# Kernel optimization log

Hardware: AMD Instinct MI355X
Metric: run time of the kernel (lower is better)

## Reference

```python
import jax, jax.numpy as jnp
import numpy as np

N = 100_000   # nodes
E = 1_250_000 # edges
D = 64        # node feature dim
H = 64        # hidden_channels
C = 10        # num_classes
G = 128       # graphs in batch


def setup_inputs() -> dict:
    key = jax.random.key(0)
    ks = jax.random.split(key, 12)
    x = jax.random.normal(ks[0], (N, D), dtype=jnp.float32)
    edge_index = jax.random.randint(ks[1], (2, E), 0, N, dtype=jnp.int64)
    batch = jnp.sort(jax.random.randint(ks[2], (N,), 0, G, dtype=jnp.int64))
    s = lambda fan_in: 1.0 / np.sqrt(fan_in)
    W1 = jax.random.normal(ks[3], (D, H), dtype=jnp.float32) * s(D)
    b1 = jnp.zeros((H,), dtype=jnp.float32)
    W2 = jax.random.normal(ks[4], (H, H), dtype=jnp.float32) * s(H)
    b2 = jnp.zeros((H,), dtype=jnp.float32)
    W3 = jax.random.normal(ks[5], (H, H), dtype=jnp.float32) * s(H)
    b3 = jnp.zeros((H,), dtype=jnp.float32)
    Wl = jax.random.normal(ks[6], (H, C), dtype=jnp.float32) * s(H)
    bl = jnp.zeros((C,), dtype=jnp.float32)
    return {"x": x, "edge_index": edge_index, "batch": batch,
            "W1": W1, "b1": b1, "W2": W2, "b2": b2,
            "W3": W3, "b3": b3, "Wl": Wl, "bl": bl}


def _gcn_conv(h, W, b, src, dst, norm, n_nodes):
    # GCNConv: out[i] = sum_{e: dst(e)=i} norm_e * (h @ W)[src(e)] + b
    h = h @ W
    msg = h[src] * norm[:, None]                       # [E+N, H]
    return jax.ops.segment_sum(msg, dst, num_segments=n_nodes) + b


def reference(x, edge_index, batch, W1, b1, W2, b2, W3, b3, Wl, bl):
    x = x.astype(jnp.float32)
    ei = edge_index.astype(jnp.int64)
    # add self-loops (as PyG gcn_norm does by default)
    loop = jnp.arange(N, dtype=ei.dtype)
    src = jnp.concatenate([ei[0], loop])
    dst = jnp.concatenate([ei[1], loop])
    # symmetric normalization: deg over targets (in-degree incl. self-loops)
    deg = jax.ops.segment_sum(jnp.ones_like(src, dtype=jnp.float32), dst,
                              num_segments=N)
    dinv = jnp.where(deg > 0, jax.lax.rsqrt(jnp.maximum(deg, 1.0)), 0.0)
    norm = dinv[src] * dinv[dst]                       # [E+N]

    h = jax.nn.relu(_gcn_conv(x, W1, b1, src, dst, norm, N))
    h = jax.nn.relu(_gcn_conv(h, W2, b2, src, dst, norm, N))
    h = _gcn_conv(h, W3, b3, src, dst, norm, N)

    # global_mean_pool over graph ids
    ones = jnp.ones((N,), dtype=jnp.float32)
    counts = jax.ops.segment_sum(ones, batch, num_segments=G)
    sums = jax.ops.segment_sum(h, batch, num_segments=G)
    pooled = sums / jnp.maximum(counts, 1.0)[:, None]  # [G, H]

    # dropout is identity in eval mode
    return pooled @ Wl + bl                            # [G, C]
```

## Files before the change

### kernel.cpp

```cpp
#include <hip/hip_runtime.h>
#include <hip/hip_bf16.h>


#define BSHIFT 7
#define BNODES (1 << BSHIFT)
#define EPB    8192
#define MAXDEG 8192
#define MAXBUCKET 32768

typedef __attribute__((ext_vector_type(8))) short bf16x8;
typedef __attribute__((ext_vector_type(4))) float f32x4;

__device__ __forceinline__ void atomAddF(float* p, float v) {
#if defined(__gfx90a__) || defined(__gfx940__) || defined(__gfx941__) || defined(__gfx942__) || defined(__gfx950__)
    unsafeAtomicAdd(p, v);
#else
    atomicAdd(p, v);
#endif
}

__device__ __forceinline__ unsigned short f2bf(float x) {
    unsigned u = __float_as_uint(x);
    u += 0x7FFFu + ((u >> 16) & 1u);
    return (unsigned short)(u >> 16);
}
__device__ __forceinline__ float bf2f(unsigned short b) {
    return __uint_as_float((unsigned)b << 16);
}

__global__ __launch_bounds__(256)
void k_bhist(const int* __restrict__ dst, int* __restrict__ cnt_all,
             int nE, int nBuckets, int binBlocks,
             const float* __restrict__ W1, const float* __restrict__ W2,
             const float* __restrict__ W3, unsigned short* __restrict__ Wt,
             float* __restrict__ pool, int poolN) {
    if (blockIdx.x >= binBlocks) {
        int li = blockIdx.x - binBlocks;
        if (li < 3) {
            const float* W = (li == 0) ? W1 : ((li == 1) ? W2 : W3);
            unsigned short* o = Wt + li * 4096;
            for (int idx = threadIdx.x; idx < 4096; idx += 256) {
                int h = idx >> 6, k = idx & 63;
                o[idx] = f2bf(W[k * 64 + h]);
            }
        } else {
            for (int i = threadIdx.x; i < poolN; i += 256) pool[i] = 0.f;
        }
        return;
    }
    __shared__ int cnt[1024];
    const int t = threadIdx.x;
    const int blk = blockIdx.x * EPB;
    for (int b = t; b < nBuckets; b += 256) cnt[b] = 0;
    __syncthreads();
#pragma unroll 4
    for (int i = 0; i < EPB / 256; i++) {
        int e = blk + i * 256 + t;
        if (e < nE) atomicAdd(&cnt[dst[e] >> BSHIFT], 1);
    }
    __syncthreads();
    for (int b = t; b < nBuckets; b += 256)
        cnt_all[(size_t)blockIdx.x * nBuckets + b] = cnt[b];
}

__global__ __launch_bounds__(256)
void k_colscan(int* __restrict__ cnt_all, int* __restrict__ bcnt,
               int nBlocks, int nBuckets) {
    const int lane = threadIdx.x & 63;
    const int b = blockIdx.x * 4 + (threadIdx.x >> 6);
    if (b >= nBuckets) return;
    int running = 0;
    for (int c = 0; c < nBlocks; c += 64) {
        int blk = c + lane;
        int v = (blk < nBlocks) ? cnt_all[(size_t)blk * nBuckets + b] : 0;
        int incl = v;
#pragma unroll
        for (int off = 1; off < 64; off <<= 1) {
            int tv = __shfl_up(incl, off);
            if (lane >= off) incl += tv;
        }
        if (blk < nBlocks) cnt_all[(size_t)blk * nBuckets + b] = running + (incl - v);
        running += __shfl(incl, 63);
    }
    if (lane == 0) bcnt[b] = running;
}

__global__ void k_bscan(const int* __restrict__ bcnt, int* __restrict__ bbase,
                        int nb, int nE) {
    __shared__ int s[256];
    const int t = threadIdx.x;
    const int base = t * 4;
    int v0 = (base + 0 < nb) ? bcnt[base + 0] : 0;
    int v1 = (base + 1 < nb) ? bcnt[base + 1] : 0;
    int v2 = (base + 2 < nb) ? bcnt[base + 2] : 0;
    int v3 = (base + 3 < nb) ? bcnt[base + 3] : 0;
    int tsum = v0 + v1 + v2 + v3;
    s[t] = tsum;
    __syncthreads();
    for (int off = 1; off < 256; off <<= 1) {
        int val = 0;
        if (t >= off) val = s[t - off];
        __syncthreads();
        if (t >= off) s[t] += val;
        __syncthreads();
    }
    int excl = s[t] - tsum;
    if (base + 0 < nb) bbase[base + 0] = excl;
    if (base + 1 < nb) bbase[base + 1] = excl + v0;
    if (base + 2 < nb) bbase[base + 2] = excl + v0 + v1;
    if (base + 3 < nb) bbase[base + 3] = excl + v0 + v1 + v2;
    if (t == 0) bbase[nb] = nE;
}

__global__ __launch_bounds__(256)
void k_bucket(const int* __restrict__ src, const int* __restrict__ dst,
              const int* __restrict__ bbase, const int* __restrict__ cnt_all,
              int* __restrict__ staging, int nE, int nBuckets) {
    __shared__ int cnt[1024];
    __shared__ int lbase[1024];
    const int t = threadIdx.x;
    const int blk = blockIdx.x * EPB;

    for (int b = t; b < nBuckets; b += 256) {
        lbase[b] = bbase[b] + cnt_all[(size_t)blockIdx.x * nBuckets + b];
        cnt[b] = 0;
    }
    __syncthreads();
#pragma unroll 4
    for (int i = 0; i < EPB / 256; i++) {
        int e = blk + i * 256 + t;
        if (e < nE) {
            int s0 = src[e], d0 = dst[e];
            int b = d0 >> BSHIFT;
            int off = atomicAdd(&cnt[b], 1);
            int pos = lbase[b] + off;
            if ((unsigned)pos < (unsigned)nE)
                staging[pos] = (s0 << BSHIFT) | (d0 & (BNODES - 1));
        }
    }
}

__global__ __launch_bounds__(256)
void k_sort(const int* __restrict__ staging, const int* __restrict__ bbase,
            int* __restrict__ csr_s, int* __restrict__ rowptr,
            int* __restrict__ rowend, float* __restrict__ dinv,
            int n, int nE) {
    __shared__ int c[BNODES];
    __shared__ int sc[BNODES];
    __shared__ int cur[BNODES];
    const int t = threadIdx.x;
    const int b = blockIdx.x;
    const int node0 = b << BSHIFT;

    int seg0 = bbase[b];
    int seg1 = bbase[b + 1];
    seg0 = max(0, min(seg0, nE));
    seg1 = max(seg0, min(seg1, nE));
    seg1 = min(seg1, seg0 + MAXBUCKET);

    if (t < BNODES) c[t] = 0;
    __syncthreads();
    for (int e = seg0 + t; e < seg1; e += 256)
        atomicAdd(&c[staging[e] & (BNODES - 1)], 1);
    __syncthreads();
    if (t < BNODES) sc[t] = c[t];
    __syncthreads();
    for (int off = 1; off < BNODES; off <<= 1) {
        int v = 0;
        if (t >= off && t < BNODES) v = sc[t - off];
        __syncthreads();
        if (t >= off && t < BNODES) sc[t] += v;
        __syncthreads();
    }
    if (t < BNODES) {
        int excl = sc[t] - c[t];
        cur[t] = excl;
        int node = node0 + t;
        if (node < n) {
            rowptr[node] = seg0 + excl;
            rowend[node] = seg0 + excl + c[t];
            dinv[node]   = rsqrtf((float)c[t] + 1.0f);
        }
    }
    __syncthreads();
    for (int e = seg0 + t; e < seg1; e += 256) {
        int p = staging[e];
        int l = p & (BNODES - 1);
        int pos = seg0 + atomicAdd(&cur[l], 1);
        if ((unsigned)pos < (unsigned)nE)
            csr_s[pos] = ((unsigned)p) >> BSHIFT;
    }
}

template<bool RELU, typename AT>
__device__ __forceinline__
void gemm_body(int bid, const AT* __restrict__ in,
               const unsigned short* __restrict__ Wt,
               const float* __restrict__ bias,
               unsigned short* __restrict__ out, int n) {
    const int lane = threadIdx.x & 63;
    const int wid  = threadIdx.x >> 6;
    const int col  = lane & 15;
    const int quad = lane >> 4;
    const int node0w = bid * 64 + wid * 16;
    const int nodeA  = node0w + col;
    const bool validA = nodeA < n;

    f32x4 zero4 = {0.f, 0.f, 0.f, 0.f};
    f32x4 acc0 = zero4, acc1 = zero4, acc2 = zero4, acc3 = zero4;

#pragma unroll
    for (int ks = 0; ks < 64; ks += 32) {
        const int kb = ks + quad * 8;
        float a[8];
        if constexpr (sizeof(AT) == 4) {
            float4 a0 = make_float4(0.f, 0.f, 0.f, 0.f);
            float4 a1 = make_float4(0.f, 0.f, 0.f, 0.f);
            if (validA) {
                a0 = *(const float4*)((const float*)in + (size_t)nodeA * 64 + kb);
                a1 = *(const float4*)((const float*)in + (size_t)nodeA * 64 + kb + 4);
            }
            a[0] = a0.x; a[1] = a0.y; a[2] = a0.z; a[3] = a0.w;
            a[4] = a1.x; a[5] = a1.y; a[6] = a1.z; a[7] = a1.w;
        } else {
            ushort4 h0 = make_ushort4(0, 0, 0, 0), h1 = make_ushort4(0, 0, 0, 0);
            if (validA) {
                h0 = *(const ushort4*)((const unsigned short*)in + (size_t)nodeA * 64 + kb);
                h1 = *(const ushort4*)((const unsigned short*)in + (size_t)nodeA * 64 + kb + 4);
            }
            a[0] = bf2f(h0.x); a[1] = bf2f(h0.y); a[2] = bf2f(h0.z); a[3] = bf2f(h0.w);
            a[4] = bf2f(h1.x); a[5] = bf2f(h1.y); a[6] = bf2f(h1.z); a[7] = bf2f(h1.w);
        }
        if (RELU) {
#pragma unroll
            for (int i = 0; i < 8; i++) a[i] = fmaxf(a[i] + bias[kb + i], 0.f);
        }
        bf16x8 af;
#pragma unroll
        for (int i = 0; i < 8; i++) af[i] = (short)f2bf(a[i]);

        const bf16x8 b0f = *(const bf16x8*)(Wt + ((0 * 16 + col) * 64 + kb));
        const bf16x8 b1f = *(const bf16x8*)(Wt + ((1 * 16 + col) * 64 + kb));
        const bf16x8 b2f = *(const bf16x8*)(Wt + ((2 * 16 + col) * 64 + kb));
        const bf16x8 b3f = *(const bf16x8*)(Wt + ((3 * 16 + col) * 64 + kb));
        acc0 = __builtin_amdgcn_mfma_f32_16x16x32_bf16(af, b0f, acc0, 0, 0, 0);
        acc1 = __builtin_amdgcn_mfma_f32_16x16x32_bf16(af, b1f, acc1, 0, 0, 0);
        acc2 = __builtin_amdgcn_mfma_f32_16x16x32_bf16(af, b2f, acc2, 0, 0, 0);
        acc3 = __builtin_amdgcn_mfma_f32_16x16x32_bf16(af, b3f, acc3, 0, 0, 0);
    }

#pragma unroll
    for (int r = 0; r < 4; r++) {
        int nn = node0w + quad * 4 + r;
        if (nn < n) {
            size_t base = (size_t)nn * 64 + col;
            out[base +  0] = f2bf(acc0[r]);
            out[base + 16] = f2bf(acc1[r]);
            out[base + 32] = f2bf(acc2[r]);
            out[base + 48] = f2bf(acc3[r]);
        }
    }
}

template<bool RELU, typename AT>
__global__ __launch_bounds__(256)
void k_gemm(const AT* __restrict__ in, const unsigned short* __restrict__ Wt,
            const float* __restrict__ bias, unsigned short* __restrict__ out, int n) {
    gemm_body<RELU, AT>(blockIdx.x, in, Wt, bias, out, n);
}

__global__ __launch_bounds__(256)
void k_wfgemm1(const int* __restrict__ csr_s, const float* __restrict__ dinv,
               float* __restrict__ csr_w, int nE, int n, int wfB,
               const float* __restrict__ x, const unsigned short* __restrict__ Wt,
               unsigned short* __restrict__ hW) {
    if (blockIdx.x < wfB) {
        int e = blockIdx.x * 256 + threadIdx.x;
        if (e < nE) {
            int s = csr_s[e];
            s = max(0, min(s, n - 1));
            csr_w[e] = dinv[s];
        }
        return;
    }
    gemm_body<false, float>(blockIdx.x - wfB, x, Wt, nullptr, hW, n);
}

template<int LAYER>
__global__ __launch_bounds__(256)
void k_agg(const unsigned short* __restrict__ hW, const int* __restrict__ rowptr,
           const int* __restrict__ rowend, const int* __restrict__ csr_s,
           const float* __restrict__ csr_w, const float* __restrict__ dinv,
           unsigned short* __restrict__ aggb, int n, int nE) {
    const int lane = threadIdx.x & 63;
    const int wid  = threadIdx.x >> 6;
    const int nA = blockIdx.x * 8 + wid * 2;
    const int nB = nA + 1;
    if (nA >= n) return;
    const bool vB = (nB < n);

    int rowA = rowptr[nA], endA = rowend[nA];
    rowA = max(0, min(rowA, nE)); endA = max(rowA, min(endA, nE));
    endA = min(endA, rowA + MAXDEG);
    int rowB = 0, endB = 0;
    if (vB) {
        rowB = rowptr[nB]; endB = rowend[nB];
        rowB = max(0, min(rowB, nE)); endB = max(rowB, min(endB, nE));
        endB = min(endB, rowB + MAXDEG);
    }
    const float diA = dinv[nA];
    const float diB = vB ? dinv[nB] : 0.f;

    float a0 = diA * diA * bf2f(hW[(size_t)nA * 64 + lane]);
    float a1 = 0.f, a2 = 0.f, a3 = 0.f;
    float b0 = vB ? diB * diB * bf2f(hW[(size_t)nB * 64 + lane]) : 0.f;
    float b1 = 0.f, b2 = 0.f, b3 = 0.f;

    int baseA = rowA, baseB = rowB;
    while (baseA < endA || baseB < endB) {
        int mA = max(0, min(32, endA - baseA));
        int mB = max(0, min(32, endB - baseB));
        int   s_l = 0;
        float w_l = 0.f;
        if (lane < 32) {
            if (lane < mA) {
                int e = baseA + lane;
                s_l = csr_s[e];
                w_l = csr_w[e] * diA;
            }
        } else {
            int l2 = lane - 32;
            if (l2 < mB) {
                int e = baseB + l2;
                s_l = csr_s[e];
                w_l = csr_w[e] * diB;
            }
        }
        const int m = max(mA, mB);
        int j = 0;
        for (; j + 4 <= m; j += 4) {
            int   sA0 = __shfl(s_l, j),      sA1 = __shfl(s_l, j + 1);
            int   sA2 = __shfl(s_l, j + 2),  sA3 = __shfl(s_l, j + 3);
            int   sB0 = __shfl(s_l, j + 32), sB1 = __shfl(s_l, j + 33);
            int   sB2 = __shfl(s_l, j + 34), sB3 = __shfl(s_l, j + 35);
            float wA0 = __shfl(w_l, j),      wA1 = __shfl(w_l, j + 1);
            float wA2 = __shfl(w_l, j + 2),  wA3 = __shfl(w_l, j + 3);
            float wB0 = __shfl(w_l, j + 32), wB1 = __shfl(w_l, j + 33);
            float wB2 = __shfl(w_l, j + 34), wB3 = __shfl(w_l, j + 35);
            float hA0 = bf2f(hW[(size_t)sA0 * 64 + lane]);
            float hA1 = bf2f(hW[(size_t)sA1 * 64 + lane]);
            float hA2 = bf2f(hW[(size_t)sA2 * 64 + lane]);
            float hA3 = bf2f(hW[(size_t)sA3 * 64 + lane]);
            float hB0 = bf2f(hW[(size_t)sB0 * 64 + lane]);
            float hB1 = bf2f(hW[(size_t)sB1 * 64 + lane]);
            float hB2 = bf2f(hW[(size_t)sB2 * 64 + lane]);
            float hB3 = bf2f(hW[(size_t)sB3 * 64 + lane]);
            a0 += wA0 * hA0; a1 += wA1 * hA1;
            a2 += wA2 * hA2; a3 += wA3 * hA3;
            b0 += wB0 * hB0; b1 += wB1 * hB1;
            b2 += wB2 * hB2; b3 += wB3 * hB3;
        }
        for (; j < m; j++) {
            int   sA = __shfl(s_l, j);
            float wA = __shfl(w_l, j);
            int   sB = __shfl(s_l, j + 32);
            float wB = __shfl(w_l, j + 32);
            a0 += wA * bf2f(hW[(size_t)sA * 64 + lane]);
            b0 += wB * bf2f(hW[(size_t)sB * 64 + lane]);
        }
        baseA += mA;
        baseB += mB;
    }
    aggb[(size_t)nA * 64 + lane] = f2bf((a0 + a1) + (a2 + a3));
    if (vB) aggb[(size_t)nB * 64 + lane] = f2bf((b0 + b1) + (b2 + b3));
}

__global__ void k_pool(const unsigned short* __restrict__ aggb,
                       const int* __restrict__ batch,
                       float* __restrict__ pool, float* __restrict__ cnt, int n) {
    const int lane = threadIdx.x;
    const int base = blockIdx.x * 64;
    int g_cur = -1, run = 0;
    float acc = 0.f;
    for (int j = 0; j < 64; j++) {
        int node = base + j;
        if (node >= n) break;
        int g = batch[node];
        if (g != g_cur) {
            if (g_cur >= 0) {
                atomAddF(&pool[g_cur * 64 + lane], acc);
                if (lane == 0) atomAddF(&cnt[g_cur], (float)run);
            }
            g_cur = g; acc = 0.f; run = 0;
        }
        acc += bf2f(aggb[(size_t)node * 64 + lane]);
        run++;
    }
    if (g_cur >= 0) {
        atomAddF(&pool[g_cur * 64 + lane], acc);
        if (lane == 0) atomAddF(&cnt[g_cur], (float)run);
    }
}

__global__ void k_final(const float* __restrict__ pool, const float* __restrict__ cnt,
                        const float* __restrict__ b3, const float* __restrict__ Wl,
                        const float* __restrict__ bl, float* __restrict__ out) {
    __shared__ float s[64];
    const int g = blockIdx.x, t = threadIdx.x;
    float c = fmaxf(cnt[g], 1.0f);
    s[t] = pool[g * 64 + t] / c + b3[t];
    __syncthreads();
    if (t < 10) {
        float acc = bl[t];
#pragma unroll
        for (int k = 0; k < 64; k++) acc += s[k] * Wl[k * 10 + t];
        out[g * 10 + t] = acc;
    }
}

extern "C" void kernel_launch(void* const* d_in, const int* in_sizes, int n_in,
                              void* d_out, int out_size, void* d_ws, size_t ws_size,
                              hipStream_t stream) {
    const float* x   = (const float*)d_in[0];
    const int*   ei  = (const int*)d_in[1];
    const int*   bat = (const int*)d_in[2];
    const float* W1  = (const float*)d_in[3];
    const float* b1  = (const float*)d_in[4];
    const float* W2  = (const float*)d_in[5];
    const float* b2  = (const float*)d_in[6];
    const float* W3  = (const float*)d_in[7];
    const float* b3  = (const float*)d_in[8];
    const float* Wl  = (const float*)d_in[9];
    const float* bl  = (const float*)d_in[10];
    float* out = (float*)d_out;

    const int N_ = in_sizes[0] / 64;
    const int E_ = in_sizes[1] / 2;
    const int G_ = out_size / 10;
    const int NB_ = (N_ + BNODES - 1) >> BSHIFT;
    const int bin_blocks = (E_ + EPB - 1) / EPB;

    char* p = (char*)d_ws;
    int*   staging = (int*)p;   p += (size_t)E_ * 4;
    int*   csr_s  = (int*)p;    p += (size_t)E_ * 4;
    float* csr_w  = (float*)p;  p += (size_t)E_ * 4;
    unsigned short* aggb = (unsigned short*)p; p += (size_t)N_ * 64 * 2;
    unsigned short* hW   = (unsigned short*)p; p += (size_t)N_ * 64 * 2;
    float* dinv   = (float*)p;  p += (size_t)N_ * 4;
    int*   rowptr = (int*)p;    p += (size_t)N_ * 4;
    int*   rowend = (int*)p;    p += (size_t)N_ * 4;
    float* pool   = (float*)p;  p += (size_t)G_ * 64 * 4;
    float* cnt    = (float*)p;  p += (size_t)G_ * 4;
    unsigned short* Wt = (unsigned short*)p; p += 3 * 4096 * 2;
    int*   bcnt   = (int*)p;    p += (size_t)(NB_ + 1) * 4;
    int*   bbase  = (int*)p;    p += (size_t)(NB_ + 1) * 4;
    int*   cnt_all = (int*)p;   p += (size_t)bin_blocks * NB_ * 4;

    const int* srcp = ei;
    const int* dstp = ei + E_;

    k_bhist<<<bin_blocks + 4, 256, 0, stream>>>(dstp, cnt_all, E_, NB_,
                                                bin_blocks, W1, W2, W3, Wt,
                                                pool, G_ * 64 + G_);
    k_colscan<<<(NB_ + 3) / 4, 256, 0, stream>>>(cnt_all, bcnt, bin_blocks, NB_);
    k_bscan<<<1, 256, 0, stream>>>(bcnt, bbase, NB_, E_);
    k_bucket<<<bin_blocks, 256, 0, stream>>>(srcp, dstp, bbase, cnt_all,
                                             staging, E_, NB_);
    k_sort<<<NB_, 256, 0, stream>>>(staging, bbase, csr_s, rowptr, rowend,
                                    dinv, N_, E_);

    const int gemm_blocks = (N_ + 63) / 64;
    const int agg_blocks  = (N_ + 7) / 8;
    const int wf_blocks   = (E_ + 255) / 256;

    k_wfgemm1<<<wf_blocks + gemm_blocks, 256, 0, stream>>>(
        csr_s, dinv, csr_w, E_, N_, wf_blocks, x, Wt, hW);
    k_agg<1><<<agg_blocks, 256, 0, stream>>>(hW, rowptr, rowend, csr_s, csr_w,
                                             dinv, aggb, N_, E_);
    k_gemm<true, unsigned short><<<gemm_blocks, 256, 0, stream>>>(aggb, Wt + 4096,
                                                                  b1, hW, N_);
    k_agg<2><<<agg_blocks, 256, 0, stream>>>(hW, rowptr, rowend, csr_s, csr_w,
                                             dinv, aggb, N_, E_);
    k_gemm<true, unsigned short><<<gemm_blocks, 256, 0, stream>>>(aggb, Wt + 8192,
                                                                  b2, hW, N_);
    k_agg<3><<<agg_blocks, 256, 0, stream>>>(hW, rowptr, rowend, csr_s, csr_w,
                                             dinv, aggb, N_, E_);

    k_pool<<<(N_ + 63) / 64, 64, 0, stream>>>(aggb, bat, pool, cnt, N_);
    k_final<<<G_, 64, 0, stream>>>(pool, cnt, b3, Wl, bl, out);
}
```

Measured before the change: 345.9 us.

## Aggregate one node per wavefront using scalar constant-address edge loads

```diff
diff --git a/kernel.cpp b/kernel.cpp
--- a/kernel.cpp
+++ b/kernel.cpp
@@ -10,6 +10,13 @@
 
 typedef __attribute__((ext_vector_type(8))) short bf16x8;
 typedef __attribute__((ext_vector_type(4))) float f32x4;
+
+#define KAS __attribute__((address_space(4)))
+
+template <typename T>
+__device__ __forceinline__ const KAS T* kptr(const T* p) {
+    return (const KAS T*)(unsigned long long)p;
+}
 
 __device__ __forceinline__ void atomAddF(float* p, float v) {
 #if defined(__gfx90a__) || defined(__gfx940__) || defined(__gfx941__) || defined(__gfx942__) || defined(__gfx950__)
@@ -294,85 +301,48 @@
            unsigned short* __restrict__ aggb, int n, int nE) {
     const int lane = threadIdx.x & 63;
     const int wid  = threadIdx.x >> 6;
-    const int nA = blockIdx.x * 8 + wid * 2;
-    const int nB = nA + 1;
-    if (nA >= n) return;
-    const bool vB = (nB < n);
-
-    int rowA = rowptr[nA], endA = rowend[nA];
+    const int node = blockIdx.x * 4 + wid;
+    if (node >= n) return;
+
+    int rowA = __builtin_amdgcn_readfirstlane(rowptr[node]);
+    int endA = __builtin_amdgcn_readfirstlane(rowend[node]);
     rowA = max(0, min(rowA, nE)); endA = max(rowA, min(endA, nE));
     endA = min(endA, rowA + MAXDEG);
-    int rowB = 0, endB = 0;
-    if (vB) {
-        rowB = rowptr[nB]; endB = rowend[nB];
-        rowB = max(0, min(rowB, nE)); endB = max(rowB, min(endB, nE));
-        endB = min(endB, rowB + MAXDEG);
-    }
-    const float diA = dinv[nA];
-    const float diB = vB ? dinv[nB] : 0.f;
-
-    float a0 = diA * diA * bf2f(hW[(size_t)nA * 64 + lane]);
-    float a1 = 0.f, a2 = 0.f, a3 = 0.f;
-    float b0 = vB ? diB * diB * bf2f(hW[(size_t)nB * 64 + lane]) : 0.f;
-    float b1 = 0.f, b2 = 0.f, b3 = 0.f;
-
-    int baseA = rowA, baseB = rowB;
-    while (baseA < endA || baseB < endB) {
-        int mA = max(0, min(32, endA - baseA));
-        int mB = max(0, min(32, endB - baseB));
-        int   s_l = 0;
-        float w_l = 0.f;
-        if (lane < 32) {
-            if (lane < mA) {
-                int e = baseA + lane;
-                s_l = csr_s[e];
-                w_l = csr_w[e] * diA;
-            }
-        } else {
-            int l2 = lane - 32;
-            if (l2 < mB) {
-                int e = baseB + l2;
-                s_l = csr_s[e];
-                w_l = csr_w[e] * diB;
-            }
-        }
-        const int m = max(mA, mB);
-        int j = 0;
-        for (; j + 4 <= m; j += 4) {
-            int   sA0 = __shfl(s_l, j),      sA1 = __shfl(s_l, j + 1);
-            int   sA2 = __shfl(s_l, j + 2),  sA3 = __shfl(s_l, j + 3);
-            int   sB0 = __shfl(s_l, j + 32), sB1 = __shfl(s_l, j + 33);
-            int   sB2 = __shfl(s_l, j + 34), sB3 = __shfl(s_l, j + 35);
-            float wA0 = __shfl(w_l, j),      wA1 = __shfl(w_l, j + 1);
-            float wA2 = __shfl(w_l, j + 2),  wA3 = __shfl(w_l, j + 3);
-            float wB0 = __shfl(w_l, j + 32), wB1 = __shfl(w_l, j + 33);
-            float wB2 = __shfl(w_l, j + 34), wB3 = __shfl(w_l, j + 35);
-            float hA0 = bf2f(hW[(size_t)sA0 * 64 + lane]);
-            float hA1 = bf2f(hW[(size_t)sA1 * 64 + lane]);
-            float hA2 = bf2f(hW[(size_t)sA2 * 64 + lane]);
-            float hA3 = bf2f(hW[(size_t)sA3 * 64 + lane]);
-            float hB0 = bf2f(hW[(size_t)sB0 * 64 + lane]);
-            float hB1 = bf2f(hW[(size_t)sB1 * 64 + lane]);
-            float hB2 = bf2f(hW[(size_t)sB2 * 64 + lane]);
-            float hB3 = bf2f(hW[(size_t)sB3 * 64 + lane]);
-            a0 += wA0 * hA0; a1 += wA1 * hA1;
-            a2 += wA2 * hA2; a3 += wA3 * hA3;
-            b0 += wB0 * hB0; b1 += wB1 * hB1;
-            b2 += wB2 * hB2; b3 += wB3 * hB3;
-        }
-        for (; j < m; j++) {
-            int   sA = __shfl(s_l, j);
-            float wA = __shfl(w_l, j);
-            int   sB = __shfl(s_l, j + 32);
-            float wB = __shfl(w_l, j + 32);
-            a0 += wA * bf2f(hW[(size_t)sA * 64 + lane]);
-            b0 += wB * bf2f(hW[(size_t)sB * 64 + lane]);
-        }
-        baseA += mA;
-        baseB += mB;
-    }
-    aggb[(size_t)nA * 64 + lane] = f2bf((a0 + a1) + (a2 + a3));
-    if (vB) aggb[(size_t)nB * 64 + lane] = f2bf((b0 + b1) + (b2 + b3));
+    const float diA = __uint_as_float(
+        __builtin_amdgcn_readfirstlane(__float_as_uint(dinv[node])));
+
+    float acc0 = diA * bf2f(hW[(size_t)node * 64 + lane]);
+    float acc1 = 0.f, acc2 = 0.f, acc3 = 0.f;
+    const int nm1 = n - 1;
+
+    for (int b = rowA; b < endA; b += 16) {
+        const KAS int*   sp = kptr(csr_s + b);
+        const KAS float* wp = kptr(csr_w + b);
+        const int rem = endA - b;
+
+        int   sidx[16];
+        float w[16];
+#pragma unroll
+        for (int j = 0; j < 16; j++) {
+            int s = sp[j];
+            s = max(0, min(s, nm1));
+            sidx[j] = (j < rem) ? s : 0;
+            w[j]    = (j < rem) ? wp[j] : 0.f;
+        }
+        float h[16];
+#pragma unroll
+        for (int j = 0; j < 16; j++)
+            h[j] = bf2f(hW[(size_t)sidx[j] * 64 + lane]);
+#pragma unroll
+        for (int j = 0; j < 16; j += 4) {
+            acc0 += w[j]     * h[j];
+            acc1 += w[j + 1] * h[j + 1];
+            acc2 += w[j + 2] * h[j + 2];
+            acc3 += w[j + 3] * h[j + 3];
+        }
+    }
+    float r = diA * ((acc0 + acc1) + (acc2 + acc3));
+    aggb[(size_t)node * 64 + lane] = f2bf(r);
 }
 
 __global__ void k_pool(const unsigned short* __restrict__ aggb,
@@ -470,7 +440,7 @@
                                     dinv, N_, E_);
 
     const int gemm_blocks = (N_ + 63) / 64;
-    const int agg_blocks  = (N_ + 7) / 8;
+    const int agg_blocks  = (N_ + 3) / 4;
     const int wf_blocks   = (E_ + 255) / 256;
 
     k_wfgemm1<<<wf_blocks + gemm_blocks, 256, 0, stream>>>(
```

Measured after the change: 363.5 us. 1.05x slower.
